# Optimization experiments

Measured on AMD Instinct MI355X. Metric: run time of the kernel, lower is better.

Reference implementation:

```python
import jax, jax.numpy as jnp
import numpy as np

S = float(np.sqrt(2.0) / 2.0)  # rotation blend coefficient sqrt(2)/2

_PERMS = {
    1: [3, 0, 1, 6, 4, 2, 7, 8, 5],
    2: [6, 3, 0, 7, 4, 1, 8, 5, 2],
    3: [7, 6, 3, 8, 4, 0, 5, 2, 1],
    4: [8, 7, 6, 5, 4, 3, 2, 1, 0],
    5: [5, 8, 7, 2, 4, 6, 1, 0, 3],
    6: [2, 5, 8, 1, 4, 7, 0, 3, 6],
    7: [1, 2, 5, 0, 4, 8, 3, 6, 7],
}


def _blend_weight_circle(weight, r):
    # weight: [O, C, 3, 3]; r: [1, 4] SE gates. Returns [8*O, C, 9].
    O, C = weight.shape[0], weight.shape[1]
    wr = weight.reshape(O, C, 9)
    c = lambda i: wr[:, :, i:i + 1]
    f0 = S * c(0) + (1 - S) * c(1); f1 = S * c(3) + (1 - S) * c(4)
    w0 = S * f0 + (1 - S) * f1
    f2 = (1 - S) * c(1) + S * c(2); f3 = (1 - S) * c(4) + S * c(5)
    w2 = S * f2 + (1 - S) * f3
    f4 = S * c(3) + (1 - S) * c(4); f5 = S * c(6) + (1 - S) * c(7)
    w6 = (1 - S) * f4 + S * f5
    f6 = (1 - S) * c(4) + S * c(5); f7 = (1 - S) * c(7) + S * c(8)
    w8 = (1 - S) * f6 + S * f7
    base = jnp.concatenate([w0, c(1), w2, c(3), c(4), c(5), w6, c(7), w8], axis=-1)
    wc0 = base * r[0, 0] + wr * (1 - r[0, 0])
    wc1 = base[:, :, _PERMS[1]]
    wc2 = base[:, :, _PERMS[2]] * r[0, 1] + wr[:, :, _PERMS[2]] * (1 - r[0, 1])
    wc3 = base[:, :, _PERMS[3]]
    wc4 = base[:, :, _PERMS[4]] * r[0, 2] + wr[:, :, _PERMS[4]] * (1 - r[0, 2])
    wc5 = base[:, :, _PERMS[5]]
    wc6 = base[:, :, _PERMS[6]] * r[0, 3] + wr[:, :, _PERMS[6]] * (1 - r[0, 3])
    wc7 = base[:, :, _PERMS[7]]
    return jnp.concatenate([wc0, wc1, wc2, wc3, wc4, wc5, wc6, wc7], axis=0)


def _dcn_v2(inp, offset, mask, wq, bias):
    # stride=1, padding=1, dilation=1, 3x3 kernel, deformable_groups=1
    B, C, Hin, Win = inp.shape
    H, W = offset.shape[2], offset.shape[3]
    K = 9
    off = offset.reshape(B, K, 2, H, W)  # channel 2k = dy, 2k+1 = dx
    ky = jnp.repeat(jnp.arange(3), 3).astype(inp.dtype)  # k // 3
    kx = jnp.tile(jnp.arange(3), 3).astype(inp.dtype)    # k %  3
    hh = jnp.arange(H, dtype=inp.dtype)
    ww = jnp.arange(W, dtype=inp.dtype)
    # sampling positions, [B,K,H,W]
    py = hh[None, None, :, None] + ky[None, :, None, None] - 1.0 + off[:, :, 0]
    px = ww[None, None, None, :] + kx[None, :, None, None] - 1.0 + off[:, :, 1]
    y0 = jnp.floor(py); x0 = jnp.floor(px)
    ly = py - y0; lx = px - x0
    inp_flat = inp.reshape(B, C, Hin * Win)

    def gather(yi, xi):
        valid = (yi >= 0) & (yi <= Hin - 1) & (xi >= 0) & (xi <= Win - 1)
        idx = (jnp.clip(yi, 0, Hin - 1) * Win + jnp.clip(xi, 0, Win - 1)).astype(jnp.int32)
        g = jnp.take_along_axis(
            inp_flat,
            jnp.broadcast_to(idx.reshape(B, 1, K * H * W), (B, C, K * H * W)),
            axis=2,
        ).reshape(B, C, K, H, W)
        return g * valid[:, None].astype(inp.dtype)

    v00 = gather(y0, x0)
    v01 = gather(y0, x0 + 1)
    v10 = gather(y0 + 1, x0)
    v11 = gather(y0 + 1, x0 + 1)
    sampled = (((1 - ly) * (1 - lx))[:, None] * v00
               + ((1 - ly) * lx)[:, None] * v01
               + (ly * (1 - lx))[:, None] * v10
               + (ly * lx)[:, None] * v11)
    sampled = sampled * mask[:, None]  # [B,C,K,H,W]
    return jnp.einsum('ock,bckhw->bohw', wq, sampled) + bias[None, :, None, None]


def setup_inputs() -> dict:
    key = jax.random.key(0)
    ks = jax.random.split(key, 8)
    B, Cin, Cout, H, W = 2, 64, 64, 128, 128
    n = Cin * 3 * 3
    stdv = 1.0 / np.sqrt(n)
    return {
        'input': jax.random.normal(ks[0], (B, Cin, H, W), jnp.float32),
        'offset': jax.random.normal(ks[1], (B, 18, H, W), jnp.float32),
        'mask': jax.random.uniform(ks[2], (B, 9, H, W), jnp.float32),
        'w_c8': jax.random.uniform(ks[3], (B, 8, H, W), jnp.float32),
        'weight': jax.random.uniform(ks[4], (Cout, Cin, 3, 3), jnp.float32, -stdv, stdv),
        'bias': jnp.zeros((Cout * 8,), jnp.float32),
        'fc_w': jax.random.normal(ks[5], (4, Cin), jnp.float32) * (1.0 / np.sqrt(Cin)),
        'fc_b': jnp.zeros((4,), jnp.float32),
    }


def reference(input, offset, mask, w_c8, weight, bias, fc_w, fc_b):
    B = input.shape[0]
    Cout = weight.shape[0]
    # SE gate: global avg pool -> sum over batch -> fc -> sigmoid, [1,4]
    pooled = input.mean(axis=(2, 3))                       # [B, Cin]
    r = jax.nn.sigmoid(pooled.sum(axis=0, keepdims=True) @ fc_w.T + fc_b)
    wq = _blend_weight_circle(weight, r)                   # [8*Cout, Cin, 9]
    result8 = _dcn_v2(input, offset, mask, wq, bias)       # [B, 8*Cout, H, W]
    H, W = result8.shape[2], result8.shape[3]
    result8 = result8.reshape(B, 8, Cout, H, W) * w_c8[:, :, None]
    return jnp.sum(result8, axis=1)
```

## Files before the change

kernel.cpp:

```cpp
#include <hip/hip_runtime.h>
#include <hip/hip_bf16.h>
#include <math.h>

#define HWSZ 16384
#define NPIX 32768
#define ROWB 1168

typedef __attribute__((ext_vector_type(8))) short bf16x8;
typedef __attribute__((ext_vector_type(4))) float f32x4;

__device__ __forceinline__ unsigned pk2(float x, float y) {
    __hip_bfloat16 bx = __float2bfloat16(x), by = __float2bfloat16(y);
    unsigned short ux, uy;
    __builtin_memcpy(&ux, &bx, 2);
    __builtin_memcpy(&uy, &by, 2);
    return (unsigned)ux | ((unsigned)uy << 16);
}

__global__ __launch_bounds__(256) void k_nhwc(const float* __restrict__ inp,
                                              __hip_bfloat16* __restrict__ inb,
                                              float* __restrict__ pooled) {
    __shared__ float ls[64 * 65];
    const int tid = threadIdx.x;
    const int p0  = blockIdx.x * 64;
    const int b   = p0 >> 14;
    const int sp0 = p0 & (HWSZ - 1);

    {
        int px = tid & 63, cg = tid >> 6;
        const float* ip = inp + (size_t)b * 64 * HWSZ + sp0 + px;
#pragma unroll
        for (int i = 0; i < 16; i++) {
            int c = cg * 16 + i;
            ls[px * 65 + c] = ip[(size_t)c * HWSZ];
        }
    }
    __syncthreads();
    if (tid < 64) {
        float s = 0.f;
#pragma unroll 8
        for (int q = 0; q < 64; q++) s += ls[q * 65 + tid];
        atomicAdd(&pooled[b * 64 + tid], s);
    }
    for (int g = tid; g < 512; g += 256) {
        int gpx = g >> 3, oct = g & 7;
        const float* src = &ls[gpx * 65 + oct * 8];
        uint4 d;
        d.x = pk2(src[0], src[1]);
        d.y = pk2(src[2], src[3]);
        d.z = pk2(src[4], src[5]);
        d.w = pk2(src[6], src[7]);
        *(uint4*)((char*)inb + (size_t)p0 * 128 + g * 16) = d;
    }
}

__global__ void k_r(const float* __restrict__ pooled,
                    const float* __restrict__ fc_w,
                    const float* __restrict__ fc_b,
                    float* __restrict__ alpha) {
    int c = threadIdx.x;
    float s = (pooled[c] + pooled[64 + c]) * (1.0f / 16384.0f);
#pragma unroll
    for (int j = 0; j < 4; j++) {
        float v = s * fc_w[j * 64 + c];
#pragma unroll
        for (int off = 32; off; off >>= 1) v += __shfl_down(v, off, 64);
        if (c == 0) {
            float z = v + fc_b[j];
            float r = 1.0f / (1.0f + expf(-z));
            alpha[2 * j]     = r;
            alpha[2 * j + 1] = 1.0f;
        }
    }
}

__global__ __launch_bounds__(256) void k_wfrag(const float* __restrict__ w,
                                               __hip_bfloat16* __restrict__ Afrag) {
    int i = blockIdx.x * 256 + threadIdx.x;
    int e = i & 7, l = (i >> 3) & 63, t = i >> 9;
    int ot = t / 18, s = t - ot * 18;
    int m = l & 15, quad = l >> 4;
    int o = ot * 16 + m;
    int k = s * 32 + quad * 8 + e;
    Afrag[i] = __float2bfloat16(w[o * 576 + k]);
}

__global__ __launch_bounds__(256) void k_fused(const __hip_bfloat16* __restrict__ inb,
                                               const float* __restrict__ off,
                                               const float* __restrict__ msk,
                                               const float* __restrict__ w8,
                                               const float* __restrict__ alpha,
                                               const __hip_bfloat16* __restrict__ Afrag,
                                               const float* __restrict__ bias,
                                               float* __restrict__ out) {
    __shared__ __attribute__((aligned(16))) char els[16 * ROWB];
    __shared__ float tapW[36][16];
    __shared__ int   tapIP[9][16];
    __shared__ float tapU[8][16];
    __shared__ float tapVV[4][16];

    const int tid = threadIdx.x;
    const int p0t = blockIdx.x * 16;

    if (tid < 144) {
        int px = tid & 15, k = tid >> 4;
        int p = p0t + px;
        int b = p >> 14, sp = p & (HWSZ - 1);
        int h = sp >> 7, w = sp & 127;
        float oy = off[(size_t)b * 18 * HWSZ + (2 * k) * HWSZ + sp];
        float ox = off[(size_t)b * 18 * HWSZ + (2 * k + 1) * HWSZ + sp];
        float m  = msk[(size_t)b * 9 * HWSZ + k * HWSZ + sp];
        float py  = (float)(h + k / 3 - 1) + oy;
        float px_ = (float)(w + k % 3 - 1) + ox;
        float fy = floorf(py), fx = floorf(px_);
        float ly = py - fy, lx = px_ - fx;
        int iy0 = (int)fy, ix0 = (int)fx;
        int iy1 = iy0 + 1, ix1 = ix0 + 1;
        bool vy0 = ((unsigned)iy0 < 128u), vy1 = ((unsigned)iy1 < 128u);
        bool vx0 = ((unsigned)ix0 < 128u), vx1 = ((unsigned)ix1 < 128u);
        float hy = 1.0f - ly, hx = 1.0f - lx;
        tapW[k * 4 + 0][px] = (vy0 && vx0) ? hy * hx * m : 0.0f;
        tapW[k * 4 + 1][px] = (vy0 && vx1) ? hy * lx * m : 0.0f;
        tapW[k * 4 + 2][px] = (vy1 && vx0) ? ly * hx * m : 0.0f;
        tapW[k * 4 + 3][px] = (vy1 && vx1) ? ly * lx * m : 0.0f;
        int cy0 = min(max(iy0, 0), 127), cy1 = min(max(iy1, 0), 127);
        int cx0 = min(max(ix0, 0), 127), cx1 = min(max(ix1, 0), 127);
        int dx = cx1 - cx0, dy = cy1 - cy0;
        tapIP[k][px] = (cy0 * 128 + cx0) | (dy << 14) | (dx << 15);
    }
    if (tid < 128) {
        int px = tid & 15, q = tid >> 4;
        int p = p0t + px;
        int b = p >> 14, sp = p & (HWSZ - 1);
        float x = w8[(size_t)b * 8 * HWSZ + q * HWSZ + sp];
        float a = alpha[q];
        tapU[q][px] = x * a;
        if ((q & 1) == 0) tapVV[q >> 1][px] = x * (1.0f - a);
    }
    __syncthreads();

    {
        const int qd = tid & 15;
        const int pl = tid >> 4;
        const int p  = p0t + pl;
        const int b  = p >> 14;
        const char* ib = (const char*)inb + (size_t)b * HWSZ * 128 + qd * 8;

        float sam[4][9];
#pragma unroll
        for (int k = 0; k < 9; k++) {
            int pk  = tapIP[k][pl];
            int pix = pk & 16383;
            int dy  = (pk >> 14) & 1;
            int dx  = (pk >> 15) & 1;
            int a00 = pix * 128;
            int a01 = a00 + dx * 128;
            int a10 = a00 + (dy << 14);
            int a11 = a10 + dx * 128;
            uint2 d00, d01, d10, d11;
            __builtin_memcpy(&d00, ib + a00, 8);
            __builtin_memcpy(&d01, ib + a01, 8);
            __builtin_memcpy(&d10, ib + a10, 8);
            __builtin_memcpy(&d11, ib + a11, 8);
            float w00 = tapW[k * 4 + 0][pl];
            float w01 = tapW[k * 4 + 1][pl];
            float w10 = tapW[k * 4 + 2][pl];
            float w11 = tapW[k * 4 + 3][pl];
#pragma unroll
            for (int cc = 0; cc < 4; cc++) {
                unsigned u00 = (cc & 1) ? ((cc & 2) ? d00.y & 0xffff0000u : d00.x & 0xffff0000u)
                                        : ((cc & 2) ? d00.y << 16 : d00.x << 16);
                unsigned u01 = (cc & 1) ? ((cc & 2) ? d01.y & 0xffff0000u : d01.x & 0xffff0000u)
                                        : ((cc & 2) ? d01.y << 16 : d01.x << 16);
                unsigned u10 = (cc & 1) ? ((cc & 2) ? d10.y & 0xffff0000u : d10.x & 0xffff0000u)
                                        : ((cc & 2) ? d10.y << 16 : d10.x << 16);
                unsigned u11 = (cc & 1) ? ((cc & 2) ? d11.y & 0xffff0000u : d11.x & 0xffff0000u)
                                        : ((cc & 2) ? d11.y << 16 : d11.x << 16);
                sam[cc][k] = w00 * __uint_as_float(u00) + w01 * __uint_as_float(u01) +
                             w10 * __uint_as_float(u10) + w11 * __uint_as_float(u11);
            }
        }

        float u[8], vv[4];
#pragma unroll
        for (int q = 0; q < 8; q++) u[q] = tapU[q][pl];
#pragma unroll
        for (int q = 0; q < 4; q++) vv[q] = tapVV[q][pl];

        constexpr int PINV[8][9] = {
            {0,1,2,3,4,5,6,7,8},
            {1,2,5,0,4,8,3,6,7},
            {2,5,8,1,4,7,0,3,6},
            {5,8,7,2,4,6,1,0,3},
            {8,7,6,5,4,3,2,1,0},
            {7,6,3,8,4,0,5,2,1},
            {6,3,0,7,4,1,8,5,2},
            {3,0,1,6,4,2,7,8,5}};
        const float SA = 0.5f, SB = 0.20710678f, SC = 0.08578644f;

        float ev[36];
#pragma unroll
        for (int cc = 0; cc < 4; cc++) {
            const float* sm = sam[cc];
            float A[9], Bv[9];
#pragma unroll
            for (int t = 0; t < 9; t++) {
                float a = 0.f, bb = 0.f;
#pragma unroll
                for (int q = 0; q < 8; q++) a += u[q] * sm[PINV[q][t]];
#pragma unroll
                for (int i = 0; i < 4; i++) bb += vv[i] * sm[PINV[2 * i][t]];
                A[t] = a; Bv[t] = bb;
            }
            float* E = ev + cc * 9;
            E[0] = SA * A[0] + Bv[0];
            E[1] = A[1] + SB * (A[0] + A[2]) + Bv[1];
            E[2] = SA * A[2] + Bv[2];
            E[3] = A[3] + SB * (A[0] + A[6]) + Bv[3];
            E[4] = A[4] + SC * (A[0] + A[2] + A[6] + A[8]) + Bv[4];
            E[5] = A[5] + SB * (A[2] + A[8]) + Bv[5];
            E[6] = SA * A[6] + Bv[6];
            E[7] = A[7] + SB * (A[6] + A[8]) + Bv[7];
            E[8] = SA * A[8] + Bv[8];
        }
        char* dst = els + pl * ROWB + qd * 72;
#pragma unroll
        for (int i = 0; i < 9; i++) {
            uint2 d;
            d.x = pk2(ev[4 * i + 0], ev[4 * i + 1]);
            d.y = pk2(ev[4 * i + 2], ev[4 * i + 3]);
            *(uint2*)(dst + i * 8) = d;
        }
    }
    __syncthreads();

    const int l    = tid & 63;
    const int wv   = tid >> 6;
    const int pl16 = l & 15;
    const int quad = l >> 4;

    const bf16x8* Ap = (const bf16x8*)Afrag;
    const char*   Bp = els + pl16 * ROWB + quad * 16;

    f32x4 acc = (f32x4){0.f, 0.f, 0.f, 0.f};
    size_t ai = (size_t)(wv * 18) * 64 + l;
#pragma unroll 3
    for (int s = 0; s < 18; s++) {
        bf16x8 av = Ap[ai + (size_t)s * 64];
        bf16x8 bv = *(const bf16x8*)(Bp + s * 64);
        acc = __builtin_amdgcn_mfma_f32_16x16x32_bf16(av, bv, acc, 0, 0, 0);
    }

    const int pp  = p0t + pl16;
    const int bb  = pp >> 14;
    const int spp = pp & (HWSZ - 1);
    float w8v[8];
#pragma unroll
    for (int q = 0; q < 8; q++) w8v[q] = w8[(size_t)bb * 8 * HWSZ + q * HWSZ + spp];

#pragma unroll
    for (int r = 0; r < 4; r++) {
        int o = wv * 16 + quad * 4 + r;
        float bv = 0.f;
#pragma unroll
        for (int q = 0; q < 8; q++) bv += w8v[q] * bias[q * 64 + o];
        out[(size_t)(bb * 64 + o) * HWSZ + spp] = acc[r] + bv;
    }
}

extern "C" void kernel_launch(void* const* d_in, const int* in_sizes, int n_in,
                              void* d_out, int out_size, void* d_ws, size_t ws_size,
                              hipStream_t stream) {
    const float* input  = (const float*)d_in[0];
    const float* offset = (const float*)d_in[1];
    const float* mask   = (const float*)d_in[2];
    const float* w_c8   = (const float*)d_in[3];
    const float* weight = (const float*)d_in[4];
    const float* bias   = (const float*)d_in[5];
    const float* fc_w   = (const float*)d_in[6];
    const float* fc_b   = (const float*)d_in[7];
    float* out = (float*)d_out;
    float* wsf = (float*)d_ws;

    __hip_bfloat16* Afrag = (__hip_bfloat16*)wsf;
    float* pooled = wsf + 18432;
    float* alpha  = wsf + 18560;
    __hip_bfloat16* inb = (__hip_bfloat16*)(wsf + 18576);

    hipMemsetAsync(pooled, 0, 128 * sizeof(float), stream);
    k_nhwc<<<dim3(512), dim3(256), 0, stream>>>(input, inb, pooled);
    k_r<<<dim3(1), dim3(64), 0, stream>>>(pooled, fc_w, fc_b, alpha);
    k_wfrag<<<dim3(144), dim3(256), 0, stream>>>(weight, Afrag);
    k_fused<<<dim3(2048), dim3(256), 0, stream>>>(inb, offset, mask, w_c8,
                                                  alpha, Afrag, bias, out);
}
```

Measured before the change: 122.6 us.

## Fuse prep kernels, compute SE gate in-block, double pixels per block

Measured after the change: 136.3 us. +11.2%, slower.

```diff
diff --git a/kernel.cpp b/kernel.cpp
--- a/kernel.cpp
+++ b/kernel.cpp
@@ -15,6 +15,23 @@
     __builtin_memcpy(&ux, &bx, 2);
     __builtin_memcpy(&uy, &by, 2);
     return (unsigned)ux | ((unsigned)uy << 16);
+}
+
+__global__ __launch_bounds__(256) void k_prep(const float* __restrict__ w,
+                                              __hip_bfloat16* __restrict__ Afrag,
+                                              float* __restrict__ pooled) {
+    int blk = blockIdx.x, tid = threadIdx.x;
+    if (blk < 144) {
+        int i = blk * 256 + tid;
+        int e = i & 7, l = (i >> 3) & 63, t = i >> 9;
+        int ot = t / 18, s = t - ot * 18;
+        int m = l & 15, quad = l >> 4;
+        int o = ot * 16 + m;
+        int k = s * 32 + quad * 8 + e;
+        Afrag[i] = __float2bfloat16(w[o * 576 + k]);
+    } else {
+        if (tid < 128) pooled[tid] = 0.f;
+    }
 }
 
 __global__ __launch_bounds__(256) void k_nhwc(const float* __restrict__ inp,
@@ -54,56 +71,28 @@
     }
 }
 
-__global__ void k_r(const float* __restrict__ pooled,
-                    const float* __restrict__ fc_w,
-                    const float* __restrict__ fc_b,
-                    float* __restrict__ alpha) {
-    int c = threadIdx.x;
-    float s = (pooled[c] + pooled[64 + c]) * (1.0f / 16384.0f);
-#pragma unroll
-    for (int j = 0; j < 4; j++) {
-        float v = s * fc_w[j * 64 + c];
-#pragma unroll
-        for (int off = 32; off; off >>= 1) v += __shfl_down(v, off, 64);
-        if (c == 0) {
-            float z = v + fc_b[j];
-            float r = 1.0f / (1.0f + expf(-z));
-            alpha[2 * j]     = r;
-            alpha[2 * j + 1] = 1.0f;
-        }
-    }
-}
-
-__global__ __launch_bounds__(256) void k_wfrag(const float* __restrict__ w,
-                                               __hip_bfloat16* __restrict__ Afrag) {
-    int i = blockIdx.x * 256 + threadIdx.x;
-    int e = i & 7, l = (i >> 3) & 63, t = i >> 9;
-    int ot = t / 18, s = t - ot * 18;
-    int m = l & 15, quad = l >> 4;
-    int o = ot * 16 + m;
-    int k = s * 32 + quad * 8 + e;
-    Afrag[i] = __float2bfloat16(w[o * 576 + k]);
-}
-
 __global__ __launch_bounds__(256) void k_fused(const __hip_bfloat16* __restrict__ inb,
                                                const float* __restrict__ off,
                                                const float* __restrict__ msk,
                                                const float* __restrict__ w8,
-                                               const float* __restrict__ alpha,
+                                               const float* __restrict__ pooled,
+                                               const float* __restrict__ fc_w,
+                                               const float* __restrict__ fc_b,
                                                const __hip_bfloat16* __restrict__ Afrag,
                                                const float* __restrict__ bias,
                                                float* __restrict__ out) {
-    __shared__ __attribute__((aligned(16))) char els[16 * ROWB];
-    __shared__ float tapW[36][16];
-    __shared__ int   tapIP[9][16];
-    __shared__ float tapU[8][16];
-    __shared__ float tapVV[4][16];
+    __shared__ __attribute__((aligned(16))) char els[32 * ROWB];
+    __shared__ float tapW[36][32];
+    __shared__ int   tapIP[9][32];
+    __shared__ float tapU[8][32];
+    __shared__ float tapVV[4][32];
+    __shared__ float aLDS[8];
 
     const int tid = threadIdx.x;
-    const int p0t = blockIdx.x * 16;
-
-    if (tid < 144) {
-        int px = tid & 15, k = tid >> 4;
+    const int p0t = blockIdx.x * 32;
+
+    for (int it = tid; it < 288; it += 256) {
+        int px = it & 31, k = it >> 5;
         int p = p0t + px;
         int b = p >> 14, sp = p & (HWSZ - 1);
         int h = sp >> 7, w = sp & 127;
@@ -128,12 +117,29 @@
         int dx = cx1 - cx0, dy = cy1 - cy0;
         tapIP[k][px] = (cy0 * 128 + cx0) | (dy << 14) | (dx << 15);
     }
-    if (tid < 128) {
-        int px = tid & 15, q = tid >> 4;
+    if (tid < 64) {
+        int c = tid;
+        float s = (pooled[c] + pooled[64 + c]) * (1.0f / 16384.0f);
+#pragma unroll
+        for (int j = 0; j < 4; j++) {
+            float v = s * fc_w[j * 64 + c];
+#pragma unroll
+            for (int o2 = 32; o2; o2 >>= 1) v += __shfl_down(v, o2, 64);
+            if (c == 0) {
+                float z = v + fc_b[j];
+                aLDS[2 * j]     = 1.0f / (1.0f + expf(-z));
+                aLDS[2 * j + 1] = 1.0f;
+            }
+        }
+    }
+    __syncthreads();
+
+    {
+        int px = tid & 31, q = tid >> 5;
         int p = p0t + px;
         int b = p >> 14, sp = p & (HWSZ - 1);
         float x = w8[(size_t)b * 8 * HWSZ + q * HWSZ + sp];
-        float a = alpha[q];
+        float a = aLDS[q];
         tapU[q][px] = x * a;
         if ((q & 1) == 0) tapVV[q >> 1][px] = x * (1.0f - a);
     }
@@ -141,52 +147,6 @@
 
     {
         const int qd = tid & 15;
-        const int pl = tid >> 4;
-        const int p  = p0t + pl;
-        const int b  = p >> 14;
-        const char* ib = (const char*)inb + (size_t)b * HWSZ * 128 + qd * 8;
-
-        float sam[4][9];
-#pragma unroll
-        for (int k = 0; k < 9; k++) {
-            int pk  = tapIP[k][pl];
-            int pix = pk & 16383;
-            int dy  = (pk >> 14) & 1;
-            int dx  = (pk >> 15) & 1;
-            int a00 = pix * 128;
-            int a01 = a00 + dx * 128;
-            int a10 = a00 + (dy << 14);
-            int a11 = a10 + dx * 128;
-            uint2 d00, d01, d10, d11;
-            __builtin_memcpy(&d00, ib + a00, 8);
-            __builtin_memcpy(&d01, ib + a01, 8);
-            __builtin_memcpy(&d10, ib + a10, 8);
-            __builtin_memcpy(&d11, ib + a11, 8);
-            float w00 = tapW[k * 4 + 0][pl];
-            float w01 = tapW[k * 4 + 1][pl];
-            float w10 = tapW[k * 4 + 2][pl];
-            float w11 = tapW[k * 4 + 3][pl];
-#pragma unroll
-            for (int cc = 0; cc < 4; cc++) {
-                unsigned u00 = (cc & 1) ? ((cc & 2) ? d00.y & 0xffff0000u : d00.x & 0xffff0000u)
-                                        : ((cc & 2) ? d00.y << 16 : d00.x << 16);
-                unsigned u01 = (cc & 1) ? ((cc & 2) ? d01.y & 0xffff0000u : d01.x & 0xffff0000u)
-                                        : ((cc & 2) ? d01.y << 16 : d01.x << 16);
-                unsigned u10 = (cc & 1) ? ((cc & 2) ? d10.y & 0xffff0000u : d10.x & 0xffff0000u)
-                                        : ((cc & 2) ? d10.y << 16 : d10.x << 16);
-                unsigned u11 = (cc & 1) ? ((cc & 2) ? d11.y & 0xffff0000u : d11.x & 0xffff0000u)
-                                        : ((cc & 2) ? d11.y << 16 : d11.x << 16);
-                sam[cc][k] = w00 * __uint_as_float(u00) + w01 * __uint_as_float(u01) +
-                             w10 * __uint_as_float(u10) + w11 * __uint_as_float(u11);
-            }
-        }
-
-        float u[8], vv[4];
-#pragma unroll
-        for (int q = 0; q < 8; q++) u[q] = tapU[q][pl];
-#pragma unroll
-        for (int q = 0; q < 4; q++) vv[q] = tapVV[q][pl];
-
         constexpr int PINV[8][9] = {
             {0,1,2,3,4,5,6,7,8},
             {1,2,5,0,4,8,3,6,7},
@@ -198,73 +158,130 @@
             {3,0,1,6,4,2,7,8,5}};
         const float SA = 0.5f, SB = 0.20710678f, SC = 0.08578644f;
 
-        float ev[36];
-#pragma unroll
-        for (int cc = 0; cc < 4; cc++) {
-            const float* sm = sam[cc];
-            float A[9], Bv[9];
-#pragma unroll
-            for (int t = 0; t < 9; t++) {
-                float a = 0.f, bb = 0.f;
-#pragma unroll
-                for (int q = 0; q < 8; q++) a += u[q] * sm[PINV[q][t]];
-#pragma unroll
-                for (int i = 0; i < 4; i++) bb += vv[i] * sm[PINV[2 * i][t]];
-                A[t] = a; Bv[t] = bb;
+#pragma unroll 1
+        for (int ph = 0; ph < 2; ph++) {
+            const int pl = (tid >> 4) + ph * 16;
+            const int p  = p0t + pl;
+            const int b  = p >> 14;
+            const char* ib = (const char*)inb + (size_t)b * HWSZ * 128 + qd * 8;
+
+            float sam[4][9];
+#pragma unroll
+            for (int k = 0; k < 9; k++) {
+                int pk  = tapIP[k][pl];
+                int pix = pk & 16383;
+                int dy  = (pk >> 14) & 1;
+                int dx  = (pk >> 15) & 1;
+                int a00 = pix * 128;
+                int a01 = a00 + dx * 128;
+                int a10 = a00 + (dy << 14);
+                int a11 = a10 + dx * 128;
+                uint2 d00, d01, d10, d11;
+                __builtin_memcpy(&d00, ib + a00, 8);
+                __builtin_memcpy(&d01, ib + a01, 8);
+                __builtin_memcpy(&d10, ib + a10, 8);
+                __builtin_memcpy(&d11, ib + a11, 8);
+                float w00 = tapW[k * 4 + 0][pl];
+                float w01 = tapW[k * 4 + 1][pl];
+                float w10 = tapW[k * 4 + 2][pl];
+                float w11 = tapW[k * 4 + 3][pl];
+#pragma unroll
+                for (int cc = 0; cc < 4; cc++) {
+                    unsigned u00 = (cc & 1) ? ((cc & 2) ? d00.y & 0xffff0000u : d00.x & 0xffff0000u)
+                                            : ((cc & 2) ? d00.y << 16 : d00.x << 16);
+                    unsigned u01 = (cc & 1) ? ((cc & 2) ? d01.y & 0xffff0000u : d01.x & 0xffff0000u)
+                                            : ((cc & 2) ? d01.y << 16 : d01.x << 16);
+                    unsigned u10 = (cc & 1) ? ((cc & 2) ? d10.y & 0xffff0000u : d10.x & 0xffff0000u)
+                                            : ((cc & 2) ? d10.y << 16 : d10.x << 16);
+                    unsigned u11 = (cc & 1) ? ((cc & 2) ? d11.y & 0xffff0000u : d11.x & 0xffff0000u)
+                                            : ((cc & 2) ? d11.y << 16 : d11.x << 16);
+                    sam[cc][k] = w00 * __uint_as_float(u00) + w01 * __uint_as_float(u01) +
+                                 w10 * __uint_as_float(u10) + w11 * __uint_as_float(u11);
+                }
             }
-            float* E = ev + cc * 9;
-            E[0] = SA * A[0] + Bv[0];
-            E[1] = A[1] + SB * (A[0] + A[2]) + Bv[1];
-            E[2] = SA * A[2] + Bv[2];
-            E[3] = A[3] + SB * (A[0] + A[6]) + Bv[3];
-            E[4] = A[4] + SC * (A[0] + A[2] + A[6] + A[8]) + Bv[4];
-            E[5] = A[5] + SB * (A[2] + A[8]) + Bv[5];
-            E[6] = SA * A[6] + Bv[6];
-            E[7] = A[7] + SB * (A[6] + A[8]) + Bv[7];
-            E[8] = SA * A[8] + Bv[8];
-        }
-        char* dst = els + pl * ROWB + qd * 72;
-#pragma unroll
-        for (int i = 0; i < 9; i++) {
-            uint2 d;
-            d.x = pk2(ev[4 * i + 0], ev[4 * i + 1]);
-            d.y = pk2(ev[4 * i + 2], ev[4 * i + 3]);
-            *(uint2*)(dst + i * 8) = d;
+
+            float u[8], vv[4];
+#pragma unroll
+            for (int q = 0; q < 8; q++) u[q] = tapU[q][pl];
+#pragma unroll
+            for (int q = 0; q < 4; q++) vv[q] = tapVV[q][pl];
+
+            float ev[36];
+#pragma unroll
+            for (int cc = 0; cc < 4; cc++) {
+                const float* sm = sam[cc];
+                float A[9], Bv[9];
+#pragma unroll
+                for (int t = 0; t < 9; t++) {
+                    float a = 0.f, bb = 0.f;
+#pragma unroll
+                    for (int q = 0; q < 8; q++) a += u[q] * sm[PINV[q][t]];
+#pragma unroll
+                    for (int i = 0; i < 4; i++) bb += vv[i] * sm[PINV[2 * i][t]];
+                    A[t] = a; Bv[t] = bb;
+                }
+                float* E = ev + cc * 9;
+                E[0] = SA * A[0] + Bv[0];
+                E[1] = A[1] + SB * (A[0] + A[2]) + Bv[1];
+                E[2] = SA * A[2] + Bv[2];
+                E[3] = A[3] + SB * (A[0] + A[6]) + Bv[3];
+                E[4] = A[4] + SC * (A[0] + A[2] + A[6] + A[8]) + Bv[4];
+                E[5] = A[5] + SB * (A[2] + A[8]) + Bv[5];
+                E[6] = SA * A[6] + Bv[6];
+                E[7] = A[7] + SB * (A[6] + A[8]) + Bv[7];
+                E[8] = SA * A[8] + Bv[8];
+            }
+            char* dst = els + pl * ROWB + qd * 72;
+#pragma unroll
+            for (int i = 0; i < 9; i++) {
+                uint2 d;
+                d.x = pk2(ev[4 * i + 0], ev[4 * i + 1]);
+                d.y = pk2(ev[4 * i + 2], ev[4 * i + 3]);
+                *(uint2*)(dst + i * 8) = d;
+            }
         }
     }
     __syncthreads();
 
     const int l    = tid & 63;
     const int wv   = tid >> 6;
-    const int pl16 = l & 15;
+    const int m16  = l & 15;
     const int quad = l >> 4;
 
     const bf16x8* Ap = (const bf16x8*)Afrag;
-    const char*   Bp = els + pl16 * ROWB + quad * 16;
-
-    f32x4 acc = (f32x4){0.f, 0.f, 0.f, 0.f};
+    const char*   Bp0 = els + m16 * ROWB + quad * 16;
+    const char*   Bp1 = Bp0 + 16 * ROWB;
+
+    f32x4 acc0 = (f32x4){0.f, 0.f, 0.f, 0.f};
+    f32x4 acc1 = (f32x4){0.f, 0.f, 0.f, 0.f};
     size_t ai = (size_t)(wv * 18) * 64 + l;
 #pragma unroll 3
     for (int s = 0; s < 18; s++) {
-        bf16x8 av = Ap[ai + (size_t)s * 64];
-        bf16x8 bv = *(const bf16x8*)(Bp + s * 64);
-        acc = __builtin_amdgcn_mfma_f32_16x16x32_bf16(av, bv, acc, 0, 0, 0);
-    }
-
-    const int pp  = p0t + pl16;
-    const int bb  = pp >> 14;
-    const int spp = pp & (HWSZ - 1);
-    float w8v[8];
-#pragma unroll
-    for (int q = 0; q < 8; q++) w8v[q] = w8[(size_t)bb * 8 * HWSZ + q * HWSZ + spp];
-
-#pragma unroll
-    for (int r = 0; r < 4; r++) {
-        int o = wv * 16 + quad * 4 + r;
-        float bv = 0.f;
-#pragma unroll
-        for (int q = 0; q < 8; q++) bv += w8v[q] * bias[q * 64 + o];
-        out[(size_t)(bb * 64 + o) * HWSZ + spp] = acc[r] + bv;
+        bf16x8 av  = Ap[ai + (size_t)s * 64];
+        bf16x8 bv0 = *(const bf16x8*)(Bp0 + s * 64);
+        bf16x8 bv1 = *(const bf16x8*)(Bp1 + s * 64);
+        acc0 = __builtin_amdgcn_mfma_f32_16x16x32_bf16(av, bv0, acc0, 0, 0, 0);
+        acc1 = __builtin_amdgcn_mfma_f32_16x16x32_bf16(av, bv1, acc1, 0, 0, 0);
+    }
+
+#pragma unroll
+    for (int pt = 0; pt < 2; pt++) {
+        const f32x4 acc = pt ? acc1 : acc0;
+        const int pp  = p0t + pt * 16 + m16;
+        const int bb  = pp >> 14;
+        const int spp = pp & (HWSZ - 1);
+        float w8v[8];
+#pragma unroll
+        for (int q = 0; q < 8; q++)
+            w8v[q] = w8[(size_t)bb * 8 * HWSZ + q * HWSZ + spp];
+#pragma unroll
+        for (int r = 0; r < 4; r++) {
+            int o = wv * 16 + quad * 4 + r;
+            float bv = 0.f;
+#pragma unroll
+            for (int q = 0; q < 8; q++) bv += w8v[q] * bias[q * 64 + o];
+            out[(size_t)(bb * 64 + o) * HWSZ + spp] = acc[r] + bv;
+        }
     }
 }
 
@@ -284,13 +301,11 @@
 
     __hip_bfloat16* Afrag = (__hip_bfloat16*)wsf;
     float* pooled = wsf + 18432;
-    float* alpha  = wsf + 18560;
     __hip_bfloat16* inb = (__hip_bfloat16*)(wsf + 18576);
 
-    hipMemsetAsync(pooled, 0, 128 * sizeof(float), stream);
+    k_prep<<<dim3(145), dim3(256), 0, stream>>>(weight, Afrag, pooled);
     k_nhwc<<<dim3(512), dim3(256), 0, stream>>>(input, inb, pooled);
-    k_r<<<dim3(1), dim3(64), 0, stream>>>(pooled, fc_w, fc_b, alpha);
-    k_wfrag<<<dim3(144), dim3(256), 0, stream>>>(weight, Afrag);
-    k_fused<<<dim3(2048), dim3(256), 0, stream>>>(inb, offset, mask, w_c8,
-                                                  alpha, Afrag, bias, out);
-}
+    k_fused<<<dim3(1024), dim3(256), 0, stream>>>(inb, offset, mask, w_c8,
+                                                  pooled, fc_w, fc_b,
+                                                  Afrag, bias, out);
+}
```
